# Kernel tuning notes

Measured on AMD Instinct MI355X. Metric: run time of the kernel, lower is better.

Reference implementation:

```python
import jax, jax.numpy as jnp
import numpy as np

H = 4        # no_heads
CH = 32      # per-head hidden (c_hidden)
INF = 1.0e9

def setup_inputs() -> dict:
    key = jax.random.key(0)
    ks = jax.random.split(key, 8)
    B, I, J, C = 1, 256, 256, 128
    s = 0.02
    return {
        "x": jax.random.normal(ks[0], (B, I, J, C), jnp.float32),
        "mask": jnp.ones((B, I, J), jnp.float32),
        "chunk_size": 0,
        "ln_w": jnp.ones((C,), jnp.float32),
        "ln_b": jnp.zeros((C,), jnp.float32),
        "w_tri": jax.random.normal(ks[1], (C, H), jnp.float32) * s,
        "wq": jax.random.normal(ks[2], (C, H * CH), jnp.float32) * s,
        "wk": jax.random.normal(ks[3], (C, H * CH), jnp.float32) * s,
        "wv": jax.random.normal(ks[4], (C, H * CH), jnp.float32) * s,
        "wg": jax.random.normal(ks[5], (C, H * CH), jnp.float32) * s,
        "bg": jnp.zeros((H * CH,), jnp.float32),
        "wo": jax.random.normal(ks[6], (H * CH, C), jnp.float32) * s,
        "bo": jnp.zeros((C,), jnp.float32),
    }

def _layer_norm(x, w, b, eps=1e-5):
    mu = jnp.mean(x, axis=-1, keepdims=True)
    var = jnp.mean(jnp.square(x - mu), axis=-1, keepdims=True)
    return (x - mu) * jax.lax.rsqrt(var + eps) * w + b

def reference(x, mask, chunk_size, ln_w, ln_b, w_tri, wq, wk, wv, wg, bg, wo, bo):
    # starting=True -> no transpose of (I, J)
    B, I, J, C = x.shape
    xn = _layer_norm(x, ln_w, ln_b)                                   # [B,I,J,C]
    # biases
    mask_bias = (INF * (mask - 1.0))[:, :, None, None, :]             # [B,I,1,1,J]
    tri_bias = jnp.einsum("bijc,ch->bhij", xn, w_tri)[:, None]        # [B,1,H,I,J]
    # gated multi-head attention over the J axis (per row I)
    q = (xn @ wq).reshape(B, I, J, H, CH) * (CH ** -0.5)              # [B,I,J,H,CH]
    k = (xn @ wk).reshape(B, I, J, H, CH)
    v = (xn @ wv).reshape(B, I, J, H, CH)
    scores = jnp.einsum("biqhd,bikhd->bihqk", q, k) + mask_bias + tri_bias
    a = jax.nn.softmax(scores, axis=-1)                               # [B,I,H,J,J]
    o = jnp.einsum("bihqk,bikhd->biqhd", a, v)                        # [B,I,J,H,CH]
    g = jax.nn.sigmoid(xn @ wg + bg).reshape(B, I, J, H, CH)
    o = (o * g).reshape(B, I, J, H * CH)
    return o @ wo + bo                                                # [B,I,J,C]
```

## Files before the change

### kernel.cpp

```cpp
#include <hip/hip_runtime.h>
#include <math.h>

#define NI 256
#define NJ 256
#define NC 128
#define NH 4
#define NCH 32

typedef __attribute__((ext_vector_type(8)))  __bf16        bf16x8;
typedef __attribute__((ext_vector_type(8)))  unsigned short u16x8;
typedef __attribute__((ext_vector_type(16))) float         f32x16;

__device__ __forceinline__ unsigned short f2bf(float f) {
    unsigned u = __builtin_bit_cast(unsigned, f);
    u += 0x7fffu + ((u >> 16) & 1u);
    return (unsigned short)(u >> 16);
}
__device__ __forceinline__ float bf2f(unsigned short s) {
    return __builtin_bit_cast(float, ((unsigned)s) << 16);
}
__device__ __forceinline__ f32x16 fzero16() {
    f32x16 z;
#pragma unroll
    for (int r = 0; r < 16; ++r) z[r] = 0.f;
    return z;
}
__device__ __forceinline__ f32x16 mfma16(bf16x8 a, bf16x8 b, f32x16 c) {
    return __builtin_amdgcn_mfma_f32_32x32x16_bf16(a, b, c, 0, 0, 0);
}

__global__ __launch_bounds__(256) void convert_weights(
    const float* __restrict__ wq, const float* __restrict__ wk,
    const float* __restrict__ wv, const float* __restrict__ wg,
    const float* __restrict__ wo, const float* __restrict__ w_tri,
    unsigned short* __restrict__ Wt_all, unsigned short* __restrict__ Wto,
    unsigned short* __restrict__ Wtri_pad)
{
    int id = blockIdx.x * 256 + threadIdx.x;
    if (id < 4 * 16384) {
        int m = id >> 14, r = id & 16383;
        int kk = r >> 7, c = r & 127;
        const float* W = (m == 0) ? wq : (m == 1) ? wk : (m == 2) ? wv : wg;
        Wt_all[(m * 128 + c) * 128 + kk] = f2bf(W[kk * 128 + c]);
    } else if (id < 5 * 16384) {
        int r = id - 4 * 16384;
        int kk = r >> 7, c = r & 127;
        Wto[c * 128 + kk] = f2bf(wo[kk * 128 + c]);
    } else {
        int r = id - 5 * 16384;
        int col = r >> 7, kk = r & 127;
        Wtri_pad[col * 128 + kk] = (col < NH) ? f2bf(w_tri[kk * NH + col]) : (unsigned short)0;
    }
}

#define XNP 136
__global__ __launch_bounds__(256, 2) void ln_proj_mfma(
    const float* __restrict__ x, const float* __restrict__ ln_w, const float* __restrict__ ln_b,
    const unsigned short* __restrict__ Wt_all, const unsigned short* __restrict__ Wtri_pad,
    const float* __restrict__ bg,
    unsigned short* __restrict__ q, unsigned short* __restrict__ k,
    unsigned short* __restrict__ v, unsigned short* __restrict__ g,
    float* __restrict__ tri)
{
    __shared__ unsigned short xn[64 * XNP];
    const int tid = threadIdx.x;
    const long tok0 = (long)blockIdx.x * 64;

    const int lane8 = tid & 7;
#pragma unroll
    for (int p = 0; p < 2; ++p) {
        const int t = p * 32 + (tid >> 3);
        const float4* xrow = (const float4*)(x + (tok0 + t) * NC + lane8 * 16);
        float4 xv[4];
        float s = 0.f;
#pragma unroll
        for (int u = 0; u < 4; ++u) {
            xv[u] = xrow[u];
            s += xv[u].x + xv[u].y + xv[u].z + xv[u].w;
        }
#pragma unroll
        for (int off = 4; off; off >>= 1) s += __shfl_down(s, off, 8);
        const float mu = __shfl(s, 0, 8) * (1.f / (float)NC);
        float s2 = 0.f;
#pragma unroll
        for (int u = 0; u < 4; ++u) {
            float dx;
            dx = xv[u].x - mu; s2 += dx * dx;
            dx = xv[u].y - mu; s2 += dx * dx;
            dx = xv[u].z - mu; s2 += dx * dx;
            dx = xv[u].w - mu; s2 += dx * dx;
        }
#pragma unroll
        for (int off = 4; off; off >>= 1) s2 += __shfl_down(s2, off, 8);
        const float rstd = rsqrtf(__shfl(s2, 0, 8) * (1.f / (float)NC) + 1e-5f);
#pragma unroll
        for (int u = 0; u < 4; ++u) {
            const int c = lane8 * 16 + u * 4;
            const float4 lw = *(const float4*)(ln_w + c);
            const float4 lb = *(const float4*)(ln_b + c);
            float o0 = (xv[u].x - mu) * rstd * lw.x + lb.x;
            float o1 = (xv[u].y - mu) * rstd * lw.y + lb.y;
            float o2 = (xv[u].z - mu) * rstd * lw.z + lb.z;
            float o3 = (xv[u].w - mu) * rstd * lw.w + lb.w;
            unsigned p0 = (unsigned)f2bf(o0) | ((unsigned)f2bf(o1) << 16);
            unsigned p1 = (unsigned)f2bf(o2) | ((unsigned)f2bf(o3) << 16);
            *(unsigned*)&xn[t * XNP + c]     = p0;
            *(unsigned*)&xn[t * XNP + c + 2] = p1;
        }
    }
    __syncthreads();

    const int w = tid >> 6, L = tid & 63, lh = L >> 5, lc = L & 31;
    f32x16 acc[2][4], accT[2];
#pragma unroll
    for (int mt = 0; mt < 2; ++mt) {
        accT[mt] = fzero16();
#pragma unroll
        for (int nt = 0; nt < 4; ++nt) acc[mt][nt] = fzero16();
    }

#pragma unroll
    for (int k0 = 0; k0 < 8; ++k0) {
        bf16x8 a0 = *(const bf16x8*)&xn[(lc)      * XNP + k0 * 16 + lh * 8];
        bf16x8 a1 = *(const bf16x8*)&xn[(32 + lc) * XNP + k0 * 16 + lh * 8];
#pragma unroll
        for (int nt = 0; nt < 4; ++nt) {
            const int ntile = w + 4 * nt;
            bf16x8 b = *(const bf16x8*)&Wt_all[(ntile * 32 + lc) * 128 + k0 * 16 + lh * 8];
            acc[0][nt] = mfma16(a0, b, acc[0][nt]);
            acc[1][nt] = mfma16(a1, b, acc[1][nt]);
        }
        bf16x8 bt = *(const bf16x8*)&Wtri_pad[lc * 128 + k0 * 16 + lh * 8];
        accT[0] = mfma16(a0, bt, accT[0]);
        accT[1] = mfma16(a1, bt, accT[1]);
    }

    const int a_row = (int)(tok0 >> 8);
    const int b0    = (int)(tok0 & 255);
    int rowl[16];
#pragma unroll
    for (int r = 0; r < 16; ++r) rowl[r] = (r & 3) + 8 * (r >> 2) + 4 * lh;

    const float bgv = bg[w * 32 + lc];
#pragma unroll
    for (int nt = 0; nt < 4; ++nt) {
        unsigned short* O = (nt == 0) ? q : (nt == 1) ? k : (nt == 2) ? v : g;
        unsigned short* Ob = O + (((long)a_row * NH + w) * NJ + b0) * NCH + lc;
#pragma unroll
        for (int mt = 0; mt < 2; ++mt) {
#pragma unroll
            for (int r = 0; r < 16; ++r) {
                const int row = mt * 32 + rowl[r];
                float val = acc[mt][nt][r];
                if (nt == 0) val *= 0.17677669529663689f;
                if (nt == 3) val = __builtin_amdgcn_rcpf(1.f + __expf(-(val + bgv)));
                Ob[(long)row * NCH] = f2bf(val);
            }
        }
    }
    if (lc < NH) {
        float* tb = tri + ((long)lc * NI + a_row) * NJ + b0;
#pragma unroll
        for (int mt = 0; mt < 2; ++mt)
#pragma unroll
            for (int r = 0; r < 16; ++r)
                tb[mt * 32 + rowl[r]] = accT[mt][r];
    }
}

__global__ __launch_bounds__(256) void swizzle_tri(
    const float* __restrict__ tri, float* __restrict__ tri_swz)
{
    const int h = blockIdx.x, qt = blockIdx.y;
    const int tid = threadIdx.x;
    const int lane = tid & 63, lh = lane >> 5, lc = lane & 31;
    const int ktp = tid >> 6;
#pragma unroll
    for (int s = 0; s < 2; ++s) {
        const int kt = ktp + s * 4;
        float vals[16];
#pragma unroll
        for (int r = 0; r < 16; ++r) {
            const int row = qt * 32 + (r & 3) + 8 * (r >> 2) + 4 * lh;
            vals[r] = tri[((long)h * NI + row) * NJ + kt * 32 + lc];
        }
        float* dst = tri_swz + ((((long)h * 8 + qt) * 8 + kt) * 64 + lane) * 16;
#pragma unroll
        for (int u = 0; u < 4; ++u)
            *(float4*)(dst + u * 4) = make_float4(vals[4*u], vals[4*u+1], vals[4*u+2], vals[4*u+3]);
    }
}

#define KSP 40
#define VTP 264
#define PBP 40
__global__ __launch_bounds__(256, 2) void attn_mfma(
    const unsigned short* __restrict__ q, const unsigned short* __restrict__ k,
    const unsigned short* __restrict__ v, const unsigned short* __restrict__ g,
    const float* __restrict__ tri_swz, const float* __restrict__ mask,
    unsigned short* __restrict__ og)
{
    __shared__ unsigned short Ks[256 * KSP];
    __shared__ unsigned short Vt[32 * VTP];
    __shared__ unsigned short Pb[4][32 * PBP];
    __shared__ float maskb[256];
    const int i = blockIdx.x, h = blockIdx.y, qh = blockIdx.z;
    const int tid = threadIdx.x;
    const int w = tid >> 6, L = tid & 63, lh = L >> 5, lc = L & 31;
    const long base = ((long)i * NH + h) * NJ * NCH;

#pragma unroll
    for (int it = 0; it < 4; ++it) {
        const int idx = it * 256 + tid;
        const int key = idx >> 2, c8 = (idx & 3) * 8;
        *(bf16x8*)&Ks[key * KSP + c8] = *(const bf16x8*)(k + base + key * NCH + c8);
    }
    {
        const int key = tid;
        const u16x8 r0 = *(const u16x8*)(v + base + key * NCH);
        const u16x8 r1 = *(const u16x8*)(v + base + key * NCH + 8);
        const u16x8 r2 = *(const u16x8*)(v + base + key * NCH + 16);
        const u16x8 r3 = *(const u16x8*)(v + base + key * NCH + 24);
#pragma unroll
        for (int u = 0; u < 8; ++u) {
            Vt[(u)      * VTP + key] = r0[u];
            Vt[(u + 8)  * VTP + key] = r1[u];
            Vt[(u + 16) * VTP + key] = r2[u];
            Vt[(u + 24) * VTP + key] = r3[u];
        }
    }
    maskb[tid] = 1.0e9f * (mask[i * NJ + tid] - 1.0f);
    __syncthreads();

    const int qt = qh * 4 + w;
    const int qbase = qt * 32;

    const bf16x8 a0 = *(const bf16x8*)(q + base + (qbase + lc) * NCH + lh * 8);
    const bf16x8 a1 = *(const bf16x8*)(q + base + (qbase + lc) * NCH + 16 + lh * 8);
    f32x16 S[8];
#pragma unroll
    for (int t = 0; t < 8; ++t) {
        bf16x8 b0 = *(const bf16x8*)&Ks[(t * 32 + lc) * KSP + lh * 8];
        bf16x8 b1 = *(const bf16x8*)&Ks[(t * 32 + lc) * KSP + 16 + lh * 8];
        f32x16 s = fzero16();
        s = mfma16(a0, b0, s);
        s = mfma16(a1, b1, s);
        S[t] = s;
    }

    const float* tsw = tri_swz + (((long)h * 8 + qt) * 8) * 64 * 16 + (long)L * 16;
    float ls[16];
#pragma unroll
    for (int r = 0; r < 16; ++r) ls[r] = 0.f;
#pragma unroll
    for (int t = 0; t < 8; ++t) {
        const float mb = maskb[t * 32 + lc];
        const float* tv = tsw + (long)t * 64 * 16;
        float4 tb[4];
#pragma unroll
        for (int u = 0; u < 4; ++u) tb[u] = *(const float4*)(tv + u * 4);
#pragma unroll
        for (int u = 0; u < 4; ++u) {
            const float bx[4] = {tb[u].x, tb[u].y, tb[u].z, tb[u].w};
#pragma unroll
            for (int e = 0; e < 4; ++e) {
                const int r = u * 4 + e;
                const float p = __expf(fminf(S[t][r] + mb + bx[e], 30.f));
                S[t][r] = p;
                ls[r] += p;
            }
        }
    }
#pragma unroll
    for (int d = 1; d < 32; d <<= 1)
#pragma unroll
        for (int r = 0; r < 16; ++r) ls[r] += __shfl_xor(ls[r], d, 64);

    int rowl[16];
#pragma unroll
    for (int r = 0; r < 16; ++r) rowl[r] = (r & 3) + 8 * (r >> 2) + 4 * lh;

    f32x16 O = fzero16();
    unsigned short* Pw = &Pb[w][0];
#pragma unroll
    for (int t = 0; t < 8; ++t) {
#pragma unroll
        for (int r = 0; r < 16; ++r)
            Pw[rowl[r] * PBP + lc] = f2bf(S[t][r]);
        bf16x8 pa0 = *(const bf16x8*)&Pw[lc * PBP + lh * 8];
        bf16x8 pa1 = *(const bf16x8*)&Pw[lc * PBP + 16 + lh * 8];
        bf16x8 vb0 = *(const bf16x8*)&Vt[lc * VTP + t * 32 + lh * 8];
        bf16x8 vb1 = *(const bf16x8*)&Vt[lc * VTP + t * 32 + 16 + lh * 8];
        O = mfma16(pa0, vb0, O);
        O = mfma16(pa1, vb1, O);
    }

    float rl[16];
#pragma unroll
    for (int r = 0; r < 16; ++r) rl[r] = __builtin_amdgcn_rcpf(ls[r]);
    const unsigned short* gb = g + base + (long)qbase * NCH + lc;
    unsigned short* ob = og + ((long)i * NJ + qbase) * NC + h * NCH + lc;
#pragma unroll
    for (int r = 0; r < 16; ++r) {
        const int row = rowl[r];
        const float gv = bf2f(gb[(long)row * NCH]);
        ob[(long)row * NC] = f2bf(O[r] * rl[r] * gv);
    }
}

#define OGP 136
__global__ __launch_bounds__(256, 4) void out_proj_mfma(
    const unsigned short* __restrict__ og, const unsigned short* __restrict__ Wto,
    const float* __restrict__ bo, float* __restrict__ out)
{
    __shared__ unsigned short t_og[64 * OGP];
    const int tid = threadIdx.x;
    const long tok0 = (long)blockIdx.x * 64;
#pragma unroll
    for (int it = 0; it < 4; ++it) {
        const int idx = it * 256 + tid;
        const int tk = idx >> 4, c8 = (idx & 15) * 8;
        *(bf16x8*)&t_og[tk * OGP + c8] = *(const bf16x8*)(og + (tok0 + tk) * NC + c8);
    }
    __syncthreads();

    const int w = tid >> 6, L = tid & 63, lh = L >> 5, lc = L & 31;
    f32x16 acc[2];
    acc[0] = fzero16(); acc[1] = fzero16();
#pragma unroll
    for (int k0 = 0; k0 < 8; ++k0) {
        bf16x8 a0 = *(const bf16x8*)&t_og[(lc)      * OGP + k0 * 16 + lh * 8];
        bf16x8 a1 = *(const bf16x8*)&t_og[(32 + lc) * OGP + k0 * 16 + lh * 8];
        bf16x8 b  = *(const bf16x8*)&Wto[(w * 32 + lc) * 128 + k0 * 16 + lh * 8];
        acc[0] = mfma16(a0, b, acc[0]);
        acc[1] = mfma16(a1, b, acc[1]);
    }
    const float bov = bo[w * 32 + lc];
#pragma unroll
    for (int mt = 0; mt < 2; ++mt)
#pragma unroll
        for (int r = 0; r < 16; ++r) {
            const int row = mt * 32 + (r & 3) + 8 * (r >> 2) + 4 * lh;
            out[(tok0 + row) * NC + w * 32 + lc] = acc[mt][r] + bov;
        }
}

extern "C" void kernel_launch(void* const* d_in, const int* in_sizes, int n_in,
                              void* d_out, int out_size, void* d_ws, size_t ws_size,
                              hipStream_t stream) {
    const float* x     = (const float*)d_in[0];
    const float* mask  = (const float*)d_in[1];
    const float* ln_w  = (const float*)d_in[3];
    const float* ln_b  = (const float*)d_in[4];
    const float* w_tri = (const float*)d_in[5];
    const float* wq    = (const float*)d_in[6];
    const float* wk    = (const float*)d_in[7];
    const float* wv    = (const float*)d_in[8];
    const float* wg    = (const float*)d_in[9];
    const float* bg    = (const float*)d_in[10];
    const float* wo    = (const float*)d_in[11];
    const float* bo    = (const float*)d_in[12];
    float* out = (float*)d_out;

    char* p = (char*)d_ws;
    const long TOK = (long)NI * NJ;
    const long QB  = TOK * NC * sizeof(unsigned short);
    unsigned short* q  = (unsigned short*)p; p += QB;
    unsigned short* k  = (unsigned short*)p; p += QB;
    unsigned short* v  = (unsigned short*)p; p += QB;
    unsigned short* g  = (unsigned short*)p; p += QB;
    unsigned short* og = (unsigned short*)p; p += QB;
    float* tri     = (float*)p; p += (long)NH * NI * NJ * sizeof(float);
    float* tri_swz = (float*)p; p += (long)NH * NI * NJ * sizeof(float);
    unsigned short* Wt_all   = (unsigned short*)p; p += 4 * 128 * 128 * sizeof(unsigned short);
    unsigned short* Wto      = (unsigned short*)p; p += 128 * 128 * sizeof(unsigned short);
    unsigned short* Wtri_pad = (unsigned short*)p; p += 32 * 128 * sizeof(unsigned short);

    hipLaunchKernelGGL(convert_weights, dim3(336), dim3(256), 0, stream,
                       wq, wk, wv, wg, wo, w_tri, Wt_all, Wto, Wtri_pad);
    hipLaunchKernelGGL(ln_proj_mfma, dim3(TOK / 64), dim3(256), 0, stream,
                       x, ln_w, ln_b, Wt_all, Wtri_pad, bg, q, k, v, g, tri);
    hipLaunchKernelGGL(swizzle_tri, dim3(NH, 8), dim3(256), 0, stream, tri, tri_swz);
    hipLaunchKernelGGL(attn_mfma, dim3(NI, NH, 2), dim3(256), 0, stream,
                       q, k, v, g, tri_swz, mask, og);
    hipLaunchKernelGGL(out_proj_mfma, dim3(TOK / 64), dim3(256), 0, stream,
                       og, Wto, bo, out);
}
```

Before: 193.5 us.

## Compute transposed scores so tri bias reads directly and P stays in registers

The score MFMA now takes K as the A operand and Q as the B operand, so each lane holds a key-row slice for one query. Softmax runs per tile in that layout and reads tri bias and mask with contiguous float4 loads, which removes the swizzle_tri kernel and its extra buffer. Probabilities are packed to bf16 and exchanged across lane halves with shuffles to build the PV operand, replacing the shared-memory P staging buffer. This also reduces register pressure, and launch bounds are raised to three blocks per CU. The row-sum reduction shrinks to a single shuffle, and the output is stored with vectorized writes.

```diff
diff --git a/kernel.cpp b/kernel.cpp
--- a/kernel.cpp
+++ b/kernel.cpp
@@ -9,6 +9,7 @@
 
 typedef __attribute__((ext_vector_type(8)))  __bf16        bf16x8;
 typedef __attribute__((ext_vector_type(8)))  unsigned short u16x8;
+typedef __attribute__((ext_vector_type(4)))  unsigned int   u32x4;
 typedef __attribute__((ext_vector_type(16))) float         f32x16;
 
 __device__ __forceinline__ unsigned short f2bf(float f) {
@@ -168,41 +169,16 @@
     }
 }
 
-__global__ __launch_bounds__(256) void swizzle_tri(
-    const float* __restrict__ tri, float* __restrict__ tri_swz)
-{
-    const int h = blockIdx.x, qt = blockIdx.y;
-    const int tid = threadIdx.x;
-    const int lane = tid & 63, lh = lane >> 5, lc = lane & 31;
-    const int ktp = tid >> 6;
-#pragma unroll
-    for (int s = 0; s < 2; ++s) {
-        const int kt = ktp + s * 4;
-        float vals[16];
-#pragma unroll
-        for (int r = 0; r < 16; ++r) {
-            const int row = qt * 32 + (r & 3) + 8 * (r >> 2) + 4 * lh;
-            vals[r] = tri[((long)h * NI + row) * NJ + kt * 32 + lc];
-        }
-        float* dst = tri_swz + ((((long)h * 8 + qt) * 8 + kt) * 64 + lane) * 16;
-#pragma unroll
-        for (int u = 0; u < 4; ++u)
-            *(float4*)(dst + u * 4) = make_float4(vals[4*u], vals[4*u+1], vals[4*u+2], vals[4*u+3]);
-    }
-}
-
 #define KSP 40
 #define VTP 264
-#define PBP 40
-__global__ __launch_bounds__(256, 2) void attn_mfma(
+__global__ __launch_bounds__(256, 3) void attn_mfma(
     const unsigned short* __restrict__ q, const unsigned short* __restrict__ k,
     const unsigned short* __restrict__ v, const unsigned short* __restrict__ g,
-    const float* __restrict__ tri_swz, const float* __restrict__ mask,
+    const float* __restrict__ tri, const float* __restrict__ mask,
     unsigned short* __restrict__ og)
 {
     __shared__ unsigned short Ks[256 * KSP];
     __shared__ unsigned short Vt[32 * VTP];
-    __shared__ unsigned short Pb[4][32 * PBP];
     __shared__ float maskb[256];
     const int i = blockIdx.x, h = blockIdx.y, qh = blockIdx.z;
     const int tid = threadIdx.x;
@@ -234,77 +210,71 @@
 
     const int qt = qh * 4 + w;
     const int qbase = qt * 32;
-
-    const bf16x8 a0 = *(const bf16x8*)(q + base + (qbase + lc) * NCH + lh * 8);
-    const bf16x8 a1 = *(const bf16x8*)(q + base + (qbase + lc) * NCH + 16 + lh * 8);
-    f32x16 S[8];
+    const int qrow  = qbase + lc;
+
+    const bf16x8 a0 = *(const bf16x8*)(q + base + (long)qrow * NCH + lh * 8);
+    const bf16x8 a1 = *(const bf16x8*)(q + base + (long)qrow * NCH + 16 + lh * 8);
+    const float* trirow = tri + ((long)h * NI + qrow) * NJ;
+
+    float ls = 0.f;
+    f32x16 O = fzero16();
+
 #pragma unroll
     for (int t = 0; t < 8; ++t) {
-        bf16x8 b0 = *(const bf16x8*)&Ks[(t * 32 + lc) * KSP + lh * 8];
-        bf16x8 b1 = *(const bf16x8*)&Ks[(t * 32 + lc) * KSP + 16 + lh * 8];
+        bf16x8 kb0 = *(const bf16x8*)&Ks[(t * 32 + lc) * KSP + lh * 8];
+        bf16x8 kb1 = *(const bf16x8*)&Ks[(t * 32 + lc) * KSP + 16 + lh * 8];
         f32x16 s = fzero16();
-        s = mfma16(a0, b0, s);
-        s = mfma16(a1, b1, s);
-        S[t] = s;
-    }
-
-    const float* tsw = tri_swz + (((long)h * 8 + qt) * 8) * 64 * 16 + (long)L * 16;
-    float ls[16];
-#pragma unroll
-    for (int r = 0; r < 16; ++r) ls[r] = 0.f;
-#pragma unroll
-    for (int t = 0; t < 8; ++t) {
-        const float mb = maskb[t * 32 + lc];
-        const float* tv = tsw + (long)t * 64 * 16;
-        float4 tb[4];
-#pragma unroll
-        for (int u = 0; u < 4; ++u) tb[u] = *(const float4*)(tv + u * 4);
-#pragma unroll
-        for (int u = 0; u < 4; ++u) {
-            const float bx[4] = {tb[u].x, tb[u].y, tb[u].z, tb[u].w};
-#pragma unroll
-            for (int e = 0; e < 4; ++e) {
-                const int r = u * 4 + e;
-                const float p = __expf(fminf(S[t][r] + mb + bx[e], 30.f));
-                S[t][r] = p;
-                ls[r] += p;
-            }
-        }
-    }
-#pragma unroll
-    for (int d = 1; d < 32; d <<= 1)
-#pragma unroll
-        for (int r = 0; r < 16; ++r) ls[r] += __shfl_xor(ls[r], d, 64);
-
-    int rowl[16];
-#pragma unroll
-    for (int r = 0; r < 16; ++r) rowl[r] = (r & 3) + 8 * (r >> 2) + 4 * lh;
-
-    f32x16 O = fzero16();
-    unsigned short* Pw = &Pb[w][0];
-#pragma unroll
-    for (int t = 0; t < 8; ++t) {
-#pragma unroll
-        for (int r = 0; r < 16; ++r)
-            Pw[rowl[r] * PBP + lc] = f2bf(S[t][r]);
-        bf16x8 pa0 = *(const bf16x8*)&Pw[lc * PBP + lh * 8];
-        bf16x8 pa1 = *(const bf16x8*)&Pw[lc * PBP + 16 + lh * 8];
-        bf16x8 vb0 = *(const bf16x8*)&Vt[lc * VTP + t * 32 + lh * 8];
-        bf16x8 vb1 = *(const bf16x8*)&Vt[lc * VTP + t * 32 + 16 + lh * 8];
-        O = mfma16(pa0, vb0, O);
-        O = mfma16(pa1, vb1, O);
-    }
-
-    float rl[16];
-#pragma unroll
-    for (int r = 0; r < 16; ++r) rl[r] = __builtin_amdgcn_rcpf(ls[r]);
-    const unsigned short* gb = g + base + (long)qbase * NCH + lc;
-    unsigned short* ob = og + ((long)i * NJ + qbase) * NC + h * NCH + lc;
-#pragma unroll
-    for (int r = 0; r < 16; ++r) {
-        const int row = rowl[r];
-        const float gv = bf2f(gb[(long)row * NCH]);
-        ob[(long)row * NC] = f2bf(O[r] * rl[r] * gv);
+        s = mfma16(kb0, a0, s);
+        s = mfma16(kb1, a1, s);
+
+        unsigned pk[8];
+#pragma unroll
+        for (int gg = 0; gg < 4; ++gg) {
+            const int kb = t * 32 + gg * 8 + 4 * lh;
+            const float4 tb = *(const float4*)(trirow + kb);
+            const float4 mb = *(const float4*)&maskb[kb];
+            const float p0 = __expf(fminf(s[4 * gg + 0] + tb.x + mb.x, 30.f));
+            const float p1 = __expf(fminf(s[4 * gg + 1] + tb.y + mb.y, 30.f));
+            const float p2 = __expf(fminf(s[4 * gg + 2] + tb.z + mb.z, 30.f));
+            const float p3 = __expf(fminf(s[4 * gg + 3] + tb.w + mb.w, 30.f));
+            ls += (p0 + p1) + (p2 + p3);
+            pk[2 * gg]     = (unsigned)f2bf(p0) | ((unsigned)f2bf(p1) << 16);
+            pk[2 * gg + 1] = (unsigned)f2bf(p2) | ((unsigned)f2bf(p3) << 16);
+        }
+
+#pragma unroll
+        for (int ss = 0; ss < 2; ++ss) {
+            const unsigned give0 = lh ? pk[4 * ss]     : pk[4 * ss + 2];
+            const unsigned give1 = lh ? pk[4 * ss + 1] : pk[4 * ss + 3];
+            const unsigned t0 = __shfl_xor(give0, 32);
+            const unsigned t1 = __shfl_xor(give1, 32);
+            u32x4 bw;
+            bw[0] = lh ? t0 : pk[4 * ss];
+            bw[1] = lh ? t1 : pk[4 * ss + 1];
+            bw[2] = lh ? pk[4 * ss + 2] : t0;
+            bw[3] = lh ? pk[4 * ss + 3] : t1;
+            const bf16x8 pb = __builtin_bit_cast(bf16x8, bw);
+            const bf16x8 va = *(const bf16x8*)&Vt[lc * VTP + t * 32 + ss * 16 + lh * 8];
+            O = mfma16(va, pb, O);
+        }
+    }
+
+    ls += __shfl_xor(ls, 32);
+    const float rl = __builtin_amdgcn_rcpf(ls);
+    const unsigned short* gb = g + base + (long)qrow * NCH;
+    unsigned short* ob = og + ((long)i * NJ + qrow) * NC + h * NCH;
+#pragma unroll
+    for (int gg = 0; gg < 4; ++gg) {
+        const int ch = gg * 8 + 4 * lh;
+        const ushort4 gv = *(const ushort4*)(gb + ch);
+        const float v0 = O[4 * gg + 0] * rl * bf2f(gv.x);
+        const float v1 = O[4 * gg + 1] * rl * bf2f(gv.y);
+        const float v2 = O[4 * gg + 2] * rl * bf2f(gv.z);
+        const float v3 = O[4 * gg + 3] * rl * bf2f(gv.w);
+        uint2 st;
+        st.x = (unsigned)f2bf(v0) | ((unsigned)f2bf(v1) << 16);
+        st.y = (unsigned)f2bf(v2) | ((unsigned)f2bf(v3) << 16);
+        *(uint2*)(ob + ch) = st;
     }
 }
 
@@ -370,8 +340,7 @@
     unsigned short* v  = (unsigned short*)p; p += QB;
     unsigned short* g  = (unsigned short*)p; p += QB;
     unsigned short* og = (unsigned short*)p; p += QB;
-    float* tri     = (float*)p; p += (long)NH * NI * NJ * sizeof(float);
-    float* tri_swz = (float*)p; p += (long)NH * NI * NJ * sizeof(float);
+    float* tri = (float*)p; p += (long)NH * NI * NJ * sizeof(float);
     unsigned short* Wt_all   = (unsigned short*)p; p += 4 * 128 * 128 * sizeof(unsigned short);
     unsigned short* Wto      = (unsigned short*)p; p += 128 * 128 * sizeof(unsigned short);
     unsigned short* Wtri_pad = (unsigned short*)p; p += 32 * 128 * sizeof(unsigned short);
@@ -380,9 +349,8 @@
                        wq, wk, wv, wg, wo, w_tri, Wt_all, Wto, Wtri_pad);
     hipLaunchKernelGGL(ln_proj_mfma, dim3(TOK / 64), dim3(256), 0, stream,
                        x, ln_w, ln_b, Wt_all, Wtri_pad, bg, q, k, v, g, tri);
-    hipLaunchKernelGGL(swizzle_tri, dim3(NH, 8), dim3(256), 0, stream, tri, tri_swz);
     hipLaunchKernelGGL(attn_mfma, dim3(NI, NH, 2), dim3(256), 0, stream,
-                       q, k, v, g, tri_swz, mask, og);
+                       q, k, v, g, tri, mask, og);
     hipLaunchKernelGGL(out_proj_mfma, dim3(TOK / 64), dim3(256), 0, stream,
                        og, Wto, bo, out);
 }
```

New measurement: 209.0 us. 8.0% more time.
